# Kernel optimization log

Hardware: AMD Instinct MI355X
Metric: run time of the kernel (lower is better)

The kernel has to match this reference:

```python
import jax, jax.numpy as jnp
import numpy as np

DIM = 768
HEADS = 8

def setup_inputs() -> dict:
    key = jax.random.key(0)
    k1, k2, k3, k4 = jax.random.split(key, 4)
    x = jax.random.normal(k1, (4, 2048, DIM), dtype=jnp.float32)
    # torch Linear(D, 3D, bias=False): weight [3D, D]; store transposed [D, 3D]
    W_qkv = jax.random.normal(k2, (DIM, 3 * DIM), dtype=jnp.float32) * (DIM ** -0.5)
    W_o = jax.random.normal(k3, (DIM, DIM), dtype=jnp.float32) * (DIM ** -0.5)
    b_o = jax.random.normal(k4, (DIM,), dtype=jnp.float32) * 0.01
    return {"x": x, "W_qkv": W_qkv, "W_o": W_o, "b_o": b_o}

def reference(x, W_qkv, W_o, b_o):
    B, N, D = x.shape
    H = HEADS
    dh = D // H
    scale = dh ** -0.5
    qkv = x @ W_qkv                                   # [B, N, 3D]
    qkv = qkv.reshape(B, N, 3, H, dh)
    qkv = jnp.transpose(qkv, (2, 0, 3, 1, 4))         # [3, B, H, N, dh]
    Q, K, V = qkv[0], qkv[1], qkv[2]
    scores = jnp.einsum('bhqd,bhkd->bhqk', Q, K) * scale  # [B, H, N, N]
    attn = jax.nn.softmax(scores, axis=-1)
    out = jnp.einsum('bhqk,bhkd->bhqd', attn, V)      # [B, H, N, dh]
    # Faithful to original: reshape [B,H,N,dh] -> [B,N,D] WITHOUT head transpose
    out = out.reshape(B, N, D)
    return out @ W_o + b_o
```

## Files before the change

### kernel.cpp

```cpp
#include <hip/hip_runtime.h>

typedef __attribute__((ext_vector_type(8))) short short8;
typedef __attribute__((ext_vector_type(4))) float f32x4;
typedef __attribute__((ext_vector_type(4))) _Float16 half4;
typedef __attribute__((ext_vector_type(8))) _Float16 half8;
typedef __attribute__((ext_vector_type(2))) __fp16 fp16x2;

#define B_SZ 4
#define NSEQ 2048
#define DIM  768
#define NH   8
#define DH   96

__device__ __forceinline__ unsigned short f2bf(float f) {
  unsigned int u = __float_as_uint(f);
  u += 0x7fffu + ((u >> 16) & 1u);
  return (unsigned short)(u >> 16);
}

__device__ __forceinline__ float fexp2(float x) {
#if __has_builtin(__builtin_amdgcn_exp2f)
  return __builtin_amdgcn_exp2f(x);
#else
  return exp2f(x);
#endif
}

__device__ __forceinline__ void glds16(const void* g, void* l) {
  __builtin_amdgcn_global_load_lds((const __attribute__((address_space(1))) void*)g,
                                   (__attribute__((address_space(3))) void*)l, 16, 0, 0);
}

__global__ __launch_bounds__(256) void cvt_x_kernel(const float* __restrict__ x,
                                                    unsigned short* __restrict__ xb) {
  int i = blockIdx.x * 256 + threadIdx.x;
  float4 v = ((const float4*)x)[i];
  ushort4 o;
  o.x = f2bf(v.x); o.y = f2bf(v.y); o.z = f2bf(v.z); o.w = f2bf(v.w);
  ((ushort4*)xb)[i] = o;
}

__global__ __launch_bounds__(256) void transpose_cvt_kernel(const float* __restrict__ W,
                                                            unsigned short* __restrict__ WT,
                                                            int ncols) {
  __shared__ float tile[32][33];
  int tx = threadIdx.x, ty = threadIdx.y;
  int c0 = blockIdx.x * 32;
  int r0 = blockIdx.y * 32;
#pragma unroll
  for (int i = 0; i < 4; i++)
    tile[ty + i * 8][tx] = W[(size_t)(r0 + ty + i * 8) * ncols + c0 + tx];
  __syncthreads();
#pragma unroll
  for (int i = 0; i < 4; i++)
    WT[(size_t)(c0 + ty + i * 8) * 768 + r0 + tx] = f2bf(tile[tx][ty + i * 8]);
}

template <int EPI>
__global__ __launch_bounds__(256) void gemm_bt(
    const unsigned short* __restrict__ A, const unsigned short* __restrict__ Bt,
    unsigned short* __restrict__ qo, unsigned short* __restrict__ ko,
    _Float16* __restrict__ vo, float* __restrict__ fo,
    const float* __restrict__ bias)
{
  __shared__ unsigned short As[128 * 32];
  __shared__ unsigned short Bs[128 * 32];
  const int t = threadIdx.x;
  const int w = t >> 6, lane = t & 63;
  const int l15 = lane & 15, qd = lane >> 4;
  const int m0 = blockIdx.y * 128, n0 = blockIdx.x * 128;
  const int wm = (w >> 1) * 64, wn = (w & 1) * 64;

  const int sr = lane >> 2;
  const int sc = (lane & 3) * 8;
  const unsigned short* ga = A  + (size_t)(m0 + w * 16 + sr) * DIM + sc;
  const unsigned short* gb = Bt + (size_t)(n0 + w * 16 + sr) * DIM + sc;

  f32x4 acc[4][4] = {};

  for (int k0 = 0; k0 < DIM; k0 += 32) {
    glds16(ga + k0,            &As[w * 512]);
    glds16(ga + 64 * DIM + k0, &As[(4 + w) * 512]);
    glds16(gb + k0,            &Bs[w * 512]);
    glds16(gb + 64 * DIM + k0, &Bs[(4 + w) * 512]);
    __syncthreads();
    short8 af[4], bfr[4];
#pragma unroll
    for (int i = 0; i < 4; i++)
      af[i]  = *(const short8*)&As[(wm + i * 16 + l15) * 32 + qd * 8];
#pragma unroll
    for (int i = 0; i < 4; i++)
      bfr[i] = *(const short8*)&Bs[(wn + i * 16 + l15) * 32 + qd * 8];
#pragma unroll
    for (int mi = 0; mi < 4; mi++)
#pragma unroll
      for (int ni = 0; ni < 4; ni++)
        acc[mi][ni] = __builtin_amdgcn_mfma_f32_16x16x32_bf16(af[mi], bfr[ni], acc[mi][ni], 0, 0, 0);
    __syncthreads();
  }

#pragma unroll
  for (int mi = 0; mi < 4; mi++)
#pragma unroll
    for (int ni = 0; ni < 4; ni++) {
      int rowb = m0 + wm + mi * 16 + qd * 4;
      int col  = n0 + wn + ni * 16 + l15;
      if (EPI == 0) {
        int b = rowb >> 11, n = rowb & 2047;
        int s = col / DIM;
        int rem = col - s * DIM;
        int hh = rem / DH;
        int c = rem - hh * DH;
        size_t bh = (size_t)(b * NH + hh);
        if (s == 2) {
          half4 pk;
#pragma unroll
          for (int r = 0; r < 4; r++) pk[r] = (_Float16)acc[mi][ni][r];
          *(half4*)&vo[(bh * DH + c) * NSEQ + n] = pk;
        } else if (s == 0) {
#pragma unroll
          for (int r = 0; r < 4; r++)
            qo[(bh * NSEQ + n + r) * DH + c] = f2bf(acc[mi][ni][r] * 0.1472444679f);
        } else {
#pragma unroll
          for (int r = 0; r < 4; r++)
            ko[(bh * NSEQ + n + r) * DH + c] = f2bf(acc[mi][ni][r]);
        }
      } else {
#pragma unroll
        for (int r = 0; r < 4; r++)
          fo[(size_t)(rowb + r) * DIM + col] = acc[mi][ni][r] + bias[col];
      }
    }
}

__global__ __launch_bounds__(256, 4) void flash_kernel(
    const unsigned short* __restrict__ Qb, const unsigned short* __restrict__ Kb,
    const _Float16* __restrict__ Vtb, unsigned short* __restrict__ Z)
{
  __shared__ unsigned short Ks[64 * 96];
  __shared__ _Float16 Vs[96 * 64];

  const int t = threadIdx.x, w = t >> 6, lane = t & 63;
  const int l15 = lane & 15, qd = lane >> 4;
  const int swz = (l15 >> 1) & 3;
  const int vswz = l15 & 7;
  const int qt = blockIdx.x, h = blockIdx.y, b = blockIdx.z;
  const size_t bh = (size_t)(b * NH + h);
  const unsigned short* Qg = Qb + (bh * NSEQ + (size_t)qt * 64) * DH;
  const unsigned short* Kg = Kb + bh * NSEQ * DH;
  const _Float16*       Vg = Vtb + bh * (size_t)DH * NSEQ;

  int koff[3];
#pragma unroll
  for (int i = 0; i < 3; i++) {
    int L = w * 192 + i * 64 + lane;
    int r = L / 12, c = L - r * 12;
    int fk = r >> 4, m = r & 15;
    int key = 32 * (fk & 1) + 4 * (fk >> 1) + 8 * (m >> 2) + (m & 3);
    koff[i] = key * 96 + ((c ^ ((r >> 1) & 3)) * 8);
  }
  int voff[3];
#pragma unroll
  for (int i = 0; i < 3; i++) {
    int L = i * 256 + t;
    int r = L >> 3, c = L & 7;
    voff[i] = r * NSEQ + ((c ^ (r & 7)) * 8);
  }

#pragma unroll
  for (int i = 0; i < 3; i++)
    glds16(Qg + koff[i], &Ks[w * 1536 + i * 512]);
  __syncthreads();
  short8 qa[3];
#pragma unroll
  for (int ks = 0; ks < 3; ks++)
    qa[ks] = *(const short8*)&Ks[(w * 16 + l15) * 96 + ((ks * 4 + qd) ^ swz) * 8];

  f32x4 o[7] = {};
  float mprev = -1e30f;
  const half8 onef = {(_Float16)1.f, (_Float16)1.f, (_Float16)1.f, (_Float16)1.f,
                      (_Float16)1.f, (_Float16)1.f, (_Float16)1.f, (_Float16)1.f};

  for (int kt = 0; kt < 32; kt++) {
    __syncthreads();
    const unsigned short* Kt = Kg + (size_t)kt * 64 * DH;
#pragma unroll
    for (int i = 0; i < 3; i++)
      glds16(Kt + koff[i], &Ks[w * 1536 + i * 512]);
    const _Float16* Vt = Vg + kt * 64;
#pragma unroll
    for (int i = 0; i < 3; i++)
      glds16(Vt + voff[i], &Vs[(i * 256 + w * 64) * 8]);
    __syncthreads();

    f32x4 s[4] = {};
#pragma unroll
    for (int ks = 0; ks < 3; ks++)
#pragma unroll
      for (int fk = 0; fk < 4; fk++) {
        short8 kf = *(const short8*)&Ks[(fk * 16 + l15) * 96 + ((ks * 4 + qd) ^ swz) * 8];
        s[fk] = __builtin_amdgcn_mfma_f32_16x16x32_bf16(kf, qa[ks], s[fk], 0, 0, 0);
      }

    float mx = fmaxf(fmaxf(s[0][0], s[0][1]), fmaxf(s[0][2], s[0][3]));
#pragma unroll
    for (int fk = 1; fk < 4; fk++)
      mx = fmaxf(mx, fmaxf(fmaxf(s[fk][0], s[fk][1]), fmaxf(s[fk][2], s[fk][3])));
    mx = fmaxf(mx, __shfl_xor(mx, 16, 64));
    mx = fmaxf(mx, __shfl_xor(mx, 32, 64));
    float mnew = fmaxf(mprev, mx);
    float alpha = fexp2(mprev - mnew);
    mprev = mnew;

    half4 pf[4];
#pragma unroll
    for (int fk = 0; fk < 4; fk++) {
      union { fp16x2 h2[2]; half4 h4; } u;
      u.h2[0] = __builtin_amdgcn_cvt_pkrtz(fexp2(s[fk][0] - mnew), fexp2(s[fk][1] - mnew));
      u.h2[1] = __builtin_amdgcn_cvt_pkrtz(fexp2(s[fk][2] - mnew), fexp2(s[fk][3] - mnew));
      pf[fk] = u.h4;
    }
#pragma unroll
    for (int i = 0; i < 7; i++) o[i] = o[i] * alpha;

#pragma unroll
    for (int p = 0; p < 2; p++) {
      union { half4 h4[2]; half8 h8; } bu;
      bu.h4[0] = pf[p]; bu.h4[1] = pf[p + 2];
#pragma unroll
      for (int fc = 0; fc < 6; fc++) {
        half8 vf = *(const half8*)&Vs[(fc * 16 + l15) * 64 + ((p * 4 + qd) ^ vswz) * 8];
        o[fc] = __builtin_amdgcn_mfma_f32_16x16x32_f16(vf, bu.h8, o[fc], 0, 0, 0);
      }
      o[6] = __builtin_amdgcn_mfma_f32_16x16x32_f16(onef, bu.h8, o[6], 0, 0, 0);
    }
  }

  float inv = 1.0f / o[6][0];
  int qloc = 32 * (w & 1) + 4 * (w >> 1) + 8 * (l15 >> 2) + (l15 & 3);
  int q = qt * 64 + qloc;
  size_t zbase = ((size_t)b * NSEQ + h * 256 + (q >> 3)) * DIM + (q & 7) * DH;
#pragma unroll
  for (int fc = 0; fc < 6; fc++)
#pragma unroll
    for (int r = 0; r < 4; r += 2) {
      unsigned int pkd = (unsigned int)f2bf(o[fc][r] * inv)
                       | ((unsigned int)f2bf(o[fc][r + 1] * inv) << 16);
      *(unsigned int*)&Z[zbase + fc * 16 + qd * 4 + r] = pkd;
    }
}

extern "C" void kernel_launch(void* const* d_in, const int* in_sizes, int n_in,
                              void* d_out, int out_size, void* d_ws, size_t ws_size,
                              hipStream_t stream)
{
  (void)in_sizes; (void)n_in; (void)out_size; (void)ws_size;
  const float* x    = (const float*)d_in[0];
  const float* Wqkv = (const float*)d_in[1];
  const float* Wo   = (const float*)d_in[2];
  const float* bo   = (const float*)d_in[3];
  float* out = (float*)d_out;

  unsigned short* ws    = (unsigned short*)d_ws;
  unsigned short* xb    = ws;
  unsigned short* wqkvT = xb    + (size_t)8192 * 768;
  unsigned short* woT   = wqkvT + (size_t)2304 * 768;
  unsigned short* Qw    = woT   + (size_t)768 * 768;
  unsigned short* Kw    = Qw    + (size_t)6291456;
  _Float16*       Vw    = (_Float16*)(Kw + (size_t)6291456);
  unsigned short* Zw    = (unsigned short*)(Vw + (size_t)6291456);

  cvt_x_kernel<<<6144, 256, 0, stream>>>(x, xb);
  transpose_cvt_kernel<<<dim3(72, 24), dim3(32, 8), 0, stream>>>(Wqkv, wqkvT, 2304);
  transpose_cvt_kernel<<<dim3(24, 24), dim3(32, 8), 0, stream>>>(Wo, woT, 768);
  gemm_bt<0><<<dim3(18, 64), 256, 0, stream>>>(xb, wqkvT, Qw, Kw, Vw, nullptr, nullptr);
  flash_kernel<<<dim3(32, 8, 4), 256, 0, stream>>>(Qw, Kw, Vw, Zw);
  gemm_bt<1><<<dim3(6, 64), 256, 0, stream>>>(Zw, woT, nullptr, nullptr, nullptr, out, bo);
}
```

Baseline: 240.7 us.

## Process two query fragments per wave in flash kernel and swizzle GEMM LDS

The flash attention kernel now handles 128 queries per block (32 per wave, as two 16-row fragments), so each loaded K/V tile is reused for twice as many queries and half as many blocks are launched. Q is staged through a shared buffer aliased with the K tile. Launch bounds drop to 2 blocks per SM because register use grows. Separately, the GEMM's LDS tiles get an XOR swizzle on the column chunk to reduce bank conflicts on fragment reads. The cost is fewer blocks (512) and lower occupancy, which may hurt latency hiding.

```diff
diff --git a/kernel.cpp b/kernel.cpp
--- a/kernel.cpp
+++ b/kernel.cpp
@@ -68,11 +68,12 @@
   const int t = threadIdx.x;
   const int w = t >> 6, lane = t & 63;
   const int l15 = lane & 15, qd = lane >> 4;
+  const int asw = (l15 >> 1) & 3;
   const int m0 = blockIdx.y * 128, n0 = blockIdx.x * 128;
   const int wm = (w >> 1) * 64, wn = (w & 1) * 64;
 
   const int sr = lane >> 2;
-  const int sc = (lane & 3) * 8;
+  const int sc = ((lane & 3) ^ ((sr >> 1) & 3)) * 8;
   const unsigned short* ga = A  + (size_t)(m0 + w * 16 + sr) * DIM + sc;
   const unsigned short* gb = Bt + (size_t)(n0 + w * 16 + sr) * DIM + sc;
 
@@ -87,10 +88,10 @@
     short8 af[4], bfr[4];
 #pragma unroll
     for (int i = 0; i < 4; i++)
-      af[i]  = *(const short8*)&As[(wm + i * 16 + l15) * 32 + qd * 8];
+      af[i]  = *(const short8*)&As[(wm + i * 16 + l15) * 32 + (qd ^ asw) * 8];
 #pragma unroll
     for (int i = 0; i < 4; i++)
-      bfr[i] = *(const short8*)&Bs[(wn + i * 16 + l15) * 32 + qd * 8];
+      bfr[i] = *(const short8*)&Bs[(wn + i * 16 + l15) * 32 + (qd ^ asw) * 8];
 #pragma unroll
     for (int mi = 0; mi < 4; mi++)
 #pragma unroll
@@ -134,12 +135,14 @@
     }
 }
 
-__global__ __launch_bounds__(256, 4) void flash_kernel(
+__global__ __launch_bounds__(256, 2) void flash_kernel(
     const unsigned short* __restrict__ Qb, const unsigned short* __restrict__ Kb,
     const _Float16* __restrict__ Vtb, unsigned short* __restrict__ Z)
 {
-  __shared__ unsigned short Ks[64 * 96];
-  __shared__ _Float16 Vs[96 * 64];
+  __shared__ unsigned char smem[24576];
+  unsigned short* Qs = (unsigned short*)smem;
+  unsigned short* Ks = (unsigned short*)smem;
+  _Float16*       Vs = (_Float16*)(smem + 12288);
 
   const int t = threadIdx.x, w = t >> 6, lane = t & 63;
   const int l15 = lane & 15, qd = lane >> 4;
@@ -147,10 +150,17 @@
   const int vswz = l15 & 7;
   const int qt = blockIdx.x, h = blockIdx.y, b = blockIdx.z;
   const size_t bh = (size_t)(b * NH + h);
-  const unsigned short* Qg = Qb + (bh * NSEQ + (size_t)qt * 64) * DH;
+  const unsigned short* Qg = Qb + (bh * NSEQ + (size_t)qt * 128) * DH;
   const unsigned short* Kg = Kb + bh * NSEQ * DH;
   const _Float16*       Vg = Vtb + bh * (size_t)DH * NSEQ;
 
+  int qoff[6];
+#pragma unroll
+  for (int i = 0; i < 6; i++) {
+    int L = i * 256 + t;
+    int r = L / 12, c = L - r * 12;
+    qoff[i] = r * 96 + ((c ^ ((r >> 1) & 3)) * 8);
+  }
   int koff[3];
 #pragma unroll
   for (int i = 0; i < 3; i++) {
@@ -169,16 +179,18 @@
   }
 
 #pragma unroll
-  for (int i = 0; i < 3; i++)
-    glds16(Qg + koff[i], &Ks[w * 1536 + i * 512]);
+  for (int i = 0; i < 6; i++)
+    glds16(Qg + qoff[i], &Qs[i * 2048 + w * 512]);
   __syncthreads();
-  short8 qa[3];
-#pragma unroll
-  for (int ks = 0; ks < 3; ks++)
-    qa[ks] = *(const short8*)&Ks[(w * 16 + l15) * 96 + ((ks * 4 + qd) ^ swz) * 8];
-
-  f32x4 o[7] = {};
-  float mprev = -1e30f;
+  short8 qa[2][3];
+#pragma unroll
+  for (int fq = 0; fq < 2; fq++)
+#pragma unroll
+    for (int ks = 0; ks < 3; ks++)
+      qa[fq][ks] = *(const short8*)&Qs[(w * 32 + fq * 16 + l15) * 96 + ((ks * 4 + qd) ^ swz) * 8];
+
+  f32x4 o[2][7] = {};
+  float mprev[2] = {-1e30f, -1e30f};
   const half8 onef = {(_Float16)1.f, (_Float16)1.f, (_Float16)1.f, (_Float16)1.f,
                       (_Float16)1.f, (_Float16)1.f, (_Float16)1.f, (_Float16)1.f};
 
@@ -194,61 +206,67 @@
       glds16(Vt + voff[i], &Vs[(i * 256 + w * 64) * 8]);
     __syncthreads();
 
-    f32x4 s[4] = {};
+    f32x4 s[2][4] = {};
 #pragma unroll
     for (int ks = 0; ks < 3; ks++)
 #pragma unroll
       for (int fk = 0; fk < 4; fk++) {
         short8 kf = *(const short8*)&Ks[(fk * 16 + l15) * 96 + ((ks * 4 + qd) ^ swz) * 8];
-        s[fk] = __builtin_amdgcn_mfma_f32_16x16x32_bf16(kf, qa[ks], s[fk], 0, 0, 0);
-      }
-
-    float mx = fmaxf(fmaxf(s[0][0], s[0][1]), fmaxf(s[0][2], s[0][3]));
-#pragma unroll
-    for (int fk = 1; fk < 4; fk++)
-      mx = fmaxf(mx, fmaxf(fmaxf(s[fk][0], s[fk][1]), fmaxf(s[fk][2], s[fk][3])));
-    mx = fmaxf(mx, __shfl_xor(mx, 16, 64));
-    mx = fmaxf(mx, __shfl_xor(mx, 32, 64));
-    float mnew = fmaxf(mprev, mx);
-    float alpha = fexp2(mprev - mnew);
-    mprev = mnew;
-
-    half4 pf[4];
-#pragma unroll
-    for (int fk = 0; fk < 4; fk++) {
-      union { fp16x2 h2[2]; half4 h4; } u;
-      u.h2[0] = __builtin_amdgcn_cvt_pkrtz(fexp2(s[fk][0] - mnew), fexp2(s[fk][1] - mnew));
-      u.h2[1] = __builtin_amdgcn_cvt_pkrtz(fexp2(s[fk][2] - mnew), fexp2(s[fk][3] - mnew));
-      pf[fk] = u.h4;
+        s[0][fk] = __builtin_amdgcn_mfma_f32_16x16x32_bf16(kf, qa[0][ks], s[0][fk], 0, 0, 0);
+        s[1][fk] = __builtin_amdgcn_mfma_f32_16x16x32_bf16(kf, qa[1][ks], s[1][fk], 0, 0, 0);
+      }
+
+#pragma unroll
+    for (int fq = 0; fq < 2; fq++) {
+      float mx = fmaxf(fmaxf(s[fq][0][0], s[fq][0][1]), fmaxf(s[fq][0][2], s[fq][0][3]));
+#pragma unroll
+      for (int fk = 1; fk < 4; fk++)
+        mx = fmaxf(mx, fmaxf(fmaxf(s[fq][fk][0], s[fq][fk][1]), fmaxf(s[fq][fk][2], s[fq][fk][3])));
+      mx = fmaxf(mx, __shfl_xor(mx, 16, 64));
+      mx = fmaxf(mx, __shfl_xor(mx, 32, 64));
+      float mnew = fmaxf(mprev[fq], mx);
+      float alpha = fexp2(mprev[fq] - mnew);
+      mprev[fq] = mnew;
+
+      half4 pf[4];
+#pragma unroll
+      for (int fk = 0; fk < 4; fk++) {
+        union { fp16x2 h2[2]; half4 h4; } u;
+        u.h2[0] = __builtin_amdgcn_cvt_pkrtz(fexp2(s[fq][fk][0] - mnew), fexp2(s[fq][fk][1] - mnew));
+        u.h2[1] = __builtin_amdgcn_cvt_pkrtz(fexp2(s[fq][fk][2] - mnew), fexp2(s[fq][fk][3] - mnew));
+        pf[fk] = u.h4;
+      }
+#pragma unroll
+      for (int i = 0; i < 7; i++) o[fq][i] = o[fq][i] * alpha;
+
+#pragma unroll
+      for (int p = 0; p < 2; p++) {
+        union { half4 h4[2]; half8 h8; } bu;
+        bu.h4[0] = pf[p]; bu.h4[1] = pf[p + 2];
+#pragma unroll
+        for (int fc = 0; fc < 6; fc++) {
+          half8 vf = *(const half8*)&Vs[(fc * 16 + l15) * 64 + ((p * 4 + qd) ^ vswz) * 8];
+          o[fq][fc] = __builtin_amdgcn_mfma_f32_16x16x32_f16(vf, bu.h8, o[fq][fc], 0, 0, 0);
+        }
+        o[fq][6] = __builtin_amdgcn_mfma_f32_16x16x32_f16(onef, bu.h8, o[fq][6], 0, 0, 0);
+      }
     }
-#pragma unroll
-    for (int i = 0; i < 7; i++) o[i] = o[i] * alpha;
-
-#pragma unroll
-    for (int p = 0; p < 2; p++) {
-      union { half4 h4[2]; half8 h8; } bu;
-      bu.h4[0] = pf[p]; bu.h4[1] = pf[p + 2];
-#pragma unroll
-      for (int fc = 0; fc < 6; fc++) {
-        half8 vf = *(const half8*)&Vs[(fc * 16 + l15) * 64 + ((p * 4 + qd) ^ vswz) * 8];
-        o[fc] = __builtin_amdgcn_mfma_f32_16x16x32_f16(vf, bu.h8, o[fc], 0, 0, 0);
-      }
-      o[6] = __builtin_amdgcn_mfma_f32_16x16x32_f16(onef, bu.h8, o[6], 0, 0, 0);
-    }
-  }
-
-  float inv = 1.0f / o[6][0];
-  int qloc = 32 * (w & 1) + 4 * (w >> 1) + 8 * (l15 >> 2) + (l15 & 3);
-  int q = qt * 64 + qloc;
-  size_t zbase = ((size_t)b * NSEQ + h * 256 + (q >> 3)) * DIM + (q & 7) * DH;
-#pragma unroll
-  for (int fc = 0; fc < 6; fc++)
-#pragma unroll
-    for (int r = 0; r < 4; r += 2) {
-      unsigned int pkd = (unsigned int)f2bf(o[fc][r] * inv)
-                       | ((unsigned int)f2bf(o[fc][r + 1] * inv) << 16);
-      *(unsigned int*)&Z[zbase + fc * 16 + qd * 4 + r] = pkd;
-    }
+  }
+
+#pragma unroll
+  for (int fq = 0; fq < 2; fq++) {
+    float inv = 1.0f / o[fq][6][0];
+    int q = qt * 128 + w * 32 + fq * 16 + l15;
+    size_t zbase = ((size_t)b * NSEQ + h * 256 + (q >> 3)) * DIM + (q & 7) * DH;
+#pragma unroll
+    for (int fc = 0; fc < 6; fc++)
+#pragma unroll
+      for (int r = 0; r < 4; r += 2) {
+        unsigned int pkd = (unsigned int)f2bf(o[fq][fc][r] * inv)
+                         | ((unsigned int)f2bf(o[fq][fc][r + 1] * inv) << 16);
+        *(unsigned int*)&Z[zbase + fc * 16 + qd * 4 + r] = pkd;
+      }
+  }
 }
 
 extern "C" void kernel_launch(void* const* d_in, const int* in_sizes, int n_in,
@@ -275,6 +293,6 @@
   transpose_cvt_kernel<<<dim3(72, 24), dim3(32, 8), 0, stream>>>(Wqkv, wqkvT, 2304);
   transpose_cvt_kernel<<<dim3(24, 24), dim3(32, 8), 0, stream>>>(Wo, woT, 768);
   gemm_bt<0><<<dim3(18, 64), 256, 0, stream>>>(xb, wqkvT, Qw, Kw, Vw, nullptr, nullptr);
-  flash_kernel<<<dim3(32, 8, 4), 256, 0, stream>>>(Qw, Kw, Vw, Zw);
+  flash_kernel<<<dim3(16, 8, 4), 256, 0, stream>>>(Qw, Kw, Vw, Zw);
   gemm_bt<1><<<dim3(6, 64), 256, 0, stream>>>(Zw, woT, nullptr, nullptr, nullptr, out, bo);
 }
```

Measured after the change: 226.9 us. 5.8% less time.
